# Performance work log

Measured on AMD Instinct MI355X. Metric: run time of the kernel, lower is better.

## Reference

```python
import jax, jax.numpy as jnp
import numpy as np

B, N, G = 4, 2000, 20            # images, proposals/img, gt boxes/img
C, P = 256, 7                    # ROIAlign output channels / pooled size
NUM_LABELS = 80
THR = 0.5                        # cfg.roi_threshold
NUM_SAMPLE = 512                 # cfg.roi_num_sample
POS_RATIO = 0.25                 # cfg.roi_positive_ratio
BETA = 1.0                       # cfg.smooth_l1_beta
IMG = 800.0


def _make_boxes(key, shape):
    k1, k2, k3, k4 = jax.random.split(key, 4)
    cx = jax.random.uniform(k1, shape) * IMG
    cy = jax.random.uniform(k2, shape) * IMG
    w = jax.random.uniform(k3, shape) * 192.0 + 8.0
    h = jax.random.uniform(k4, shape) * 192.0 + 8.0
    return jnp.stack([cx - w / 2, cy - h / 2, cx + w / 2, cy + h / 2], -1)


def setup_inputs() -> dict:
    key = jax.random.key(0)
    ks = jax.random.split(key, 8)
    feat_dim = C * P * P  # 12544
    return {
        "align_features": jax.random.normal(ks[0], (B * N, C, P, P), jnp.float32),
        "proposals": _make_boxes(ks[1], (B, N)),
        "gt_boxes": _make_boxes(ks[2], (B, G)),
        "gt_labels": jax.random.randint(ks[3], (B, G), 1, NUM_LABELS + 1),
        "W1": jax.random.normal(ks[4], (feat_dim, 1024), jnp.float32) * 0.01,
        "b1": jnp.zeros((1024,), jnp.float32),
        "W2": jax.random.normal(ks[5], (1024, 1024), jnp.float32) * 0.02,
        "b2": jnp.zeros((1024,), jnp.float32),
        "Wc": jax.random.normal(ks[6], (1024, NUM_LABELS + 1), jnp.float32) * 0.02,
        "bc": jnp.zeros((NUM_LABELS + 1,), jnp.float32),
        "Wb": jax.random.normal(ks[7], (1024, 4), jnp.float32) * 0.02,
        "bb": jnp.zeros((4,), jnp.float32),
    }


def _iou_matrix(p, g):
    # p: [B,N,4], g: [B,G,4] xyxy -> [B,N,G]
    x1 = jnp.maximum(p[:, :, None, 0], g[:, None, :, 0])
    y1 = jnp.maximum(p[:, :, None, 1], g[:, None, :, 1])
    x2 = jnp.minimum(p[:, :, None, 2], g[:, None, :, 2])
    y2 = jnp.minimum(p[:, :, None, 3], g[:, None, :, 3])
    inter = jnp.clip(x2 - x1, 0.0) * jnp.clip(y2 - y1, 0.0)
    ap = (p[..., 2] - p[..., 0]) * (p[..., 3] - p[..., 1])
    ag = (g[..., 2] - g[..., 0]) * (g[..., 3] - g[..., 1])
    return inter / (ap[:, :, None] + ag[:, None, :] - inter)


def _pos_to_delta(gt, p, posm):
    # Box.pos_to_delta; gt boxes are zeros for non-positives, so sanitize with posm
    pw = p[..., 2] - p[..., 0]
    ph = p[..., 3] - p[..., 1]
    pcx = p[..., 0] + 0.5 * pw
    pcy = p[..., 1] + 0.5 * ph
    gw = jnp.where(posm, gt[..., 2] - gt[..., 0], pw)
    gh = jnp.where(posm, gt[..., 3] - gt[..., 1], ph)
    gcx = jnp.where(posm, 0.5 * (gt[..., 0] + gt[..., 2]), pcx)
    gcy = jnp.where(posm, 0.5 * (gt[..., 1] + gt[..., 3]), pcy)
    dx = (gcx - pcx) / pw
    dy = (gcy - pcy) / ph
    dw = jnp.log(gw / pw)
    dh = jnp.log(gh / ph)
    return jnp.stack([dx, dy, dw, dh], -1)


def _forward(align_features, proposals, gt_boxes, gt_labels,
             W1, b1, W2, b2, Wc, bc, Wb, bb):
    # ---- labeling_proposals: IoU matrix + threshold assignment ----
    iou = _iou_matrix(proposals, gt_boxes)                 # [B,N,G]
    max_iou = iou.max(-1)
    match = iou.argmax(-1)                                 # [B,N]
    matched_lab = jnp.take_along_axis(gt_labels, match, 1)
    matched_box = jnp.take_along_axis(gt_boxes, match[..., None], 1)
    fg = max_iou > THR
    label = jnp.where(fg, matched_lab, 0)                  # [B,N]
    match_gt = jnp.where(fg[..., None], matched_box, 0.0)  # [B,N,4]

    # ---- sampling_proposals (deterministic first-k in place of randperm) ----
    num_pos = int(NUM_SAMPLE * POS_RATIO)
    num_neg = NUM_SAMPLE - num_pos
    pos = label >= 1
    neg = label == 0
    keep_p = pos & (jnp.cumsum(pos.astype(jnp.int32), 1) <= num_pos)
    keep_n = neg & (jnp.cumsum(neg.astype(jnp.int32), 1) <= num_neg)
    samp = jnp.where(keep_p, label, jnp.where(keep_n, 0, -1))  # [B,N]

    # ---- predict_scores_deltas: dense FC head ----
    x = align_features.reshape(B * N, -1)                  # [BN, 12544]
    h = jax.nn.relu(x @ W1 + b1)
    h = jax.nn.relu(h @ W2 + b2)
    probs = jax.nn.softmax(h @ Wc + bc, -1).reshape(B, N, -1)
    deltas = (h @ Wb + bb).reshape(B, N, 4)

    # ---- loss: NOTE original applies F.cross_entropy to already-softmaxed
    # scores (double softmax); replicated faithfully here. ----
    logp = jax.nn.log_softmax(probs, -1)
    tgt = jnp.clip(samp, 0)
    nll = -jnp.take_along_axis(logp, tgt[..., None], -1)[..., 0]
    valid = (samp >= 0).astype(probs.dtype)
    cls_loss = jnp.sum(nll * valid) / (B * NUM_SAMPLE)

    posm = samp > 0
    gt_d = _pos_to_delta(match_gt, proposals, posm)
    d = deltas - gt_d
    ad = jnp.abs(d)
    sl1 = jnp.where(ad < BETA, 0.5 * d * d / BETA, ad - 0.5 * BETA)
    loc_loss = jnp.sum(sl1 * posm[..., None].astype(sl1.dtype)) / (B * NUM_SAMPLE)
    return jnp.stack([cls_loss, loc_loss])


def reference(align_features, proposals, gt_boxes, gt_labels,
              W1, b1, W2, b2, Wc, bc, Wb, bb):
    return _forward(align_features, proposals, gt_boxes, gt_labels,
                    W1, b1, W2, b2, Wc, bc, Wb, bb)
```

## Files before the change

### kernel.cpp

```cpp
#include <hip/hip_runtime.h>
#include <hip/hip_bf16.h>
#include <stdint.h>

#define B_IMG 4
#define N_PROP 2000
#define G_GT 20
#define NPROP_TOT 8000
#define FEAT 12544
#define H_DIM 1024
#define NCLS 81
#define NCB 85
#define NCB_PAD 128
#define THR_IOU 0.5f
#define NUM_POS 128
#define NUM_NEG 384
#define M_SAMP 2048
#define SPLITK 4

typedef short bf16x8 __attribute__((ext_vector_type(8)));
typedef float f32x4 __attribute__((ext_vector_type(4)));

#define GLOBAL_AS __attribute__((address_space(1)))
#define LDS_AS __attribute__((address_space(3)))

__device__ __forceinline__ unsigned short f2bf(float f) {
    unsigned u = __float_as_uint(f);
    unsigned r = 0x7FFFu + ((u >> 16) & 1u);
    return (unsigned short)((u + r) >> 16);
}

__device__ __forceinline__ void async_lds16(void* lds, const void* g) {
    __builtin_amdgcn_global_load_lds((const GLOBAL_AS unsigned int*)g,
                                     (LDS_AS unsigned int*)lds, 16, 0, 0);
}

__global__ void k_sample(const float* __restrict__ prop, const float* __restrict__ gt,
                         const int* __restrict__ gtl,
                         int* __restrict__ sval, int* __restrict__ gidx,
                         float* __restrict__ gtdc, float* __restrict__ out2) {
    if (threadIdx.x == 0) { out2[0] = 0.f; out2[1] = 0.f; }
    int w = threadIdx.x >> 6;
    int lane = threadIdx.x & 63;
    for (int i = lane; i < 512; i += 64) { sval[w*512 + i] = -1; gidx[w*512 + i] = 0; }
    int run_p = 0, run_n = 0, run_s = 0;
    unsigned long long below = (1ull << lane) - 1ull;
    const float* gb_img = gt + (long)w * G_GT * 4;
    for (int c = 0; c < (N_PROP + 63) / 64; ++c) {
        int n = c * 64 + lane;
        int p = w * N_PROP + n;
        bool valid = n < N_PROP;
        int lab = 0, bi = 0;
        float px1=0, py1=0, px2=0, py2=0;
        if (valid) {
            const float* pr = prop + (long)p * 4;
            px1 = pr[0]; py1 = pr[1]; px2 = pr[2]; py2 = pr[3];
            float ap = (px2 - px1) * (py2 - py1);
            float best = -1.f;
            for (int g = 0; g < G_GT; ++g) {
                float gx1 = gb_img[g*4+0], gy1 = gb_img[g*4+1];
                float gx2 = gb_img[g*4+2], gy2 = gb_img[g*4+3];
                float iw = fmaxf(fminf(px2, gx2) - fmaxf(px1, gx1), 0.f);
                float ih = fmaxf(fminf(py2, gy2) - fmaxf(py1, gy1), 0.f);
                float inter = iw * ih;
                float ag = (gx2 - gx1) * (gy2 - gy1);
                float iou = inter / (ap + ag - inter);
                if (iou > best) { best = iou; bi = g; }
            }
            bool fg = best > THR_IOU;
            lab = fg ? gtl[w * G_GT + bi] : 0;
        }
        bool pos = valid && (lab >= 1);
        bool neg = valid && (lab == 0);
        unsigned long long mp = __ballot(pos);
        unsigned long long mn = __ballot(neg);
        int rp = run_p + __popcll(mp & below) + 1;
        int rn = run_n + __popcll(mn & below) + 1;
        int s = -1;
        if (pos && rp <= NUM_POS) s = lab;
        else if (neg && rn <= NUM_NEG) s = 0;
        run_p += __popcll(mp);
        run_n += __popcll(mn);
        bool sampled = s >= 0;
        unsigned long long ms = __ballot(sampled);
        int slot = w * 512 + run_s + __popcll(ms & below);
        run_s += __popcll(ms);
        if (sampled) {
            sval[slot] = s;
            gidx[slot] = p;
            if (s > 0) {
                const float* gb = gb_img + (long)bi * 4;
                float pw = px2 - px1, ph = py2 - py1;
                float pcx = px1 + 0.5f * pw, pcy = py1 + 0.5f * ph;
                float gw = gb[2] - gb[0], gh = gb[3] - gb[1];
                float gcx = 0.5f * (gb[0] + gb[2]), gcy = 0.5f * (gb[1] + gb[3]);
                gtdc[slot*4+0] = (gcx - pcx) / pw;
                gtdc[slot*4+1] = (gcy - pcy) / ph;
                gtdc[slot*4+2] = logf(gw / pw);
                gtdc[slot*4+3] = logf(gh / ph);
            }
        }
    }
}

__global__ void k_gather(const float* __restrict__ x, const int* __restrict__ gidx,
                         unsigned short* __restrict__ xg) {
    int row = blockIdx.x;
    const float* src = x + (long)gidx[row] * FEAT;
    unsigned short* dst = xg + (long)row * FEAT;
    for (int i = threadIdx.x * 4; i < FEAT; i += 1024) {
        float4 v = *(const float4*)(src + i);
        ushort4 o;
        o.x = f2bf(v.x); o.y = f2bf(v.y); o.z = f2bf(v.z); o.w = f2bf(v.w);
        *(ushort4*)(dst + i) = o;
    }
}

__global__ void k_transpose(const float* __restrict__ src, unsigned short* __restrict__ dst,
                            int K, int N) {
    __shared__ float tile[32][33];
    int k0 = blockIdx.x * 32;
    int n0 = blockIdx.y * 32;
    int tx = threadIdx.x & 31;
    int ty = threadIdx.x >> 5;
    for (int r = 0; r < 4; ++r)
        tile[ty + r * 8][tx] = src[(long)(k0 + ty + r * 8) * N + (n0 + tx)];
    __syncthreads();
    for (int r = 0; r < 4; ++r)
        dst[(long)(n0 + ty + r * 8) * K + (k0 + tx)] = f2bf(tile[tx][ty + r * 8]);
}

__global__ void k_build_wcb(const float* __restrict__ Wc, const float* __restrict__ bc,
                            const float* __restrict__ Wb, const float* __restrict__ bb,
                            unsigned short* __restrict__ WT, float* __restrict__ bias) {
    int idx = blockIdx.x * blockDim.x + threadIdx.x;
    if (idx >= NCB_PAD * H_DIM) return;
    int n = idx / H_DIM;
    int k = idx - n * H_DIM;
    float v = 0.f;
    if (n < NCLS) v = Wc[k * NCLS + n];
    else if (n < NCB) v = Wb[k * 4 + (n - NCLS)];
    WT[n * H_DIM + k] = f2bf(v);
    if (idx < NCB_PAD) {
        float bv = 0.f;
        if (idx < NCLS) bv = bc[idx];
        else if (idx < NCB) bv = bb[idx - NCLS];
        bias[idx] = bv;
    }
}

template<int TM, int OUT_MODE>
__global__ __launch_bounds__(256, 2)
void k_gemm(const unsigned short* __restrict__ A, const unsigned short* __restrict__ BT,
            const float* __restrict__ bias, void* __restrict__ Out,
            int M, int N, int K, int n_tiles_m, int n_tiles_n, int k_len) {
    __shared__ unsigned short As[TM * 32];
    __shared__ unsigned short Bs[128 * 32];
    const int t = threadIdx.x;
    int bid = blockIdx.x;
    const int tile_n = bid % n_tiles_n; bid /= n_tiles_n;
    const int tile_m = bid % n_tiles_m;
    const int ks = bid / n_tiles_m;
    const int m0 = tile_m * TM, n0 = tile_n * 128;
    const int w = t >> 6, lane = t & 63;
    const int wr = w >> 1, wc = w & 1;
    const int lm = lane & 15, quad = lane >> 4;
    const int rowt = t >> 2, seg = t & 3;
    const long kbase = (long)ks * k_len;

    const unsigned short* B_0 = BT + (long)(n0 + rowt) * K + kbase + seg * 8;
    const unsigned short* B_1 = BT + (long)(n0 + rowt + 64) * K + kbase + seg * 8;
    unsigned short* lB0 = &Bs[t * 8];
    unsigned short* lB1 = &Bs[(t + 256) * 8];

    const unsigned short* A_0 = nullptr;
    const unsigned short* A_1 = nullptr;
    unsigned short* lA0 = &As[t * 8];
    unsigned short* lA1 = nullptr;
    if constexpr (TM == 128) {
        A_0 = A + (long)(m0 + rowt) * K + kbase + seg * 8;
        A_1 = A + (long)(m0 + rowt + 64) * K + kbase + seg * 8;
        lA1 = &As[(t + 256) * 8];
    } else if constexpr (TM == 64) {
        A_0 = A + (long)(m0 + rowt) * K + kbase + seg * 8;
    } else {
        if (t < 128) A_0 = A + (long)(m0 + rowt) * K + kbase + seg * 8;
    }

    constexpr int MI = TM / 32;
    f32x4 acc[MI][4];
    for (int i = 0; i < MI; ++i)
        for (int j = 0; j < 4; ++j)
            for (int r = 0; r < 4; ++r) acc[i][j][r] = 0.f;

    const int KT = k_len >> 5;
    for (int kt = 0; kt < KT; ++kt) {
        async_lds16(lB0, B_0);
        async_lds16(lB1, B_1);
        B_0 += 32; B_1 += 32;
        if constexpr (TM == 128) {
            async_lds16(lA0, A_0); A_0 += 32;
            async_lds16(lA1, A_1); A_1 += 32;
        } else if constexpr (TM == 64) {
            async_lds16(lA0, A_0); A_0 += 32;
        } else {
            if (t < 128) { async_lds16(lA0, A_0); A_0 += 32; }
        }
        __syncthreads();
        bf16x8 af[MI], bfr[4];
        for (int i = 0; i < MI; ++i)
            af[i] = *(const bf16x8*)&As[(wr * (TM / 2) + i * 16 + lm) * 32 + quad * 8];
        for (int j = 0; j < 4; ++j)
            bfr[j] = *(const bf16x8*)&Bs[(wc * 64 + j * 16 + lm) * 32 + quad * 8];
        for (int i = 0; i < MI; ++i)
            for (int j = 0; j < 4; ++j)
                acc[i][j] = __builtin_amdgcn_mfma_f32_16x16x32_bf16(af[i], bfr[j], acc[i][j], 0, 0, 0);
        __syncthreads();
    }

    for (int i = 0; i < MI; ++i) {
        const int mbase = m0 + wr * (TM / 2) + i * 16 + quad * 4;
        for (int j = 0; j < 4; ++j) {
            const int n = n0 + wc * 64 + j * 16 + lm;
            float bv = 0.f;
            if constexpr (OUT_MODE != 0) bv = bias[n];
            for (int r = 0; r < 4; ++r) {
                const int m = mbase + r;
                float v = acc[i][j][r] + bv;
                if constexpr (OUT_MODE == 0) {
                    ((float*)Out)[((long)ks * M + m) * N + n] = v;
                } else if constexpr (OUT_MODE == 1) {
                    v = fmaxf(v, 0.f);
                    ((unsigned short*)Out)[(long)m * N + n] = f2bf(v);
                } else {
                    ((float*)Out)[(long)m * N + n] = v;
                }
            }
        }
    }
}

__global__ void k_reduce(const float* __restrict__ part, const float* __restrict__ b1,
                         unsigned short* __restrict__ h1) {
    const long MN = (long)M_SAMP * H_DIM;
    long i = ((long)blockIdx.x * 256 + threadIdx.x) * 4;
    float4 a = *(const float4*)(part + i);
    float4 b = *(const float4*)(part + MN + i);
    float4 c = *(const float4*)(part + 2 * MN + i);
    float4 d = *(const float4*)(part + 3 * MN + i);
    int col = (int)(i & (H_DIM - 1));
    float4 bv = *(const float4*)(b1 + col);
    ushort4 o;
    o.x = f2bf(fmaxf(a.x + b.x + c.x + d.x + bv.x, 0.f));
    o.y = f2bf(fmaxf(a.y + b.y + c.y + d.y + bv.y, 0.f));
    o.z = f2bf(fmaxf(a.z + b.z + c.z + d.z + bv.z, 0.f));
    o.w = f2bf(fmaxf(a.w + b.w + c.w + d.w + bv.w, 0.f));
    *(ushort4*)(h1 + i) = o;
}

__global__ void k_loss(const float* __restrict__ scores, const int* __restrict__ sval,
                       const float* __restrict__ gtdc, float* __restrict__ out2) {
    int i = blockIdx.x * blockDim.x + threadIdx.x;
    float cls = 0.f, loc = 0.f;
    int s = sval[i];
    if (s >= 0) {
        const float* sc = scores + (long)i * NCB_PAD;
        float mx = sc[0];
        for (int j = 1; j < NCLS; ++j) mx = fmaxf(mx, sc[j]);
        float sum = 0.f;
        for (int j = 0; j < NCLS; ++j) sum += __expf(sc[j] - mx);
        float inv = 1.f / sum;
        float m2 = -1e30f;
        for (int j = 0; j < NCLS; ++j)
            m2 = fmaxf(m2, __expf(sc[j] - mx) * inv);
        float s2 = 0.f, ptgt = 0.f;
        for (int j = 0; j < NCLS; ++j) {
            float pj = __expf(sc[j] - mx) * inv;
            s2 += __expf(pj - m2);
            if (j == s) ptgt = pj;
        }
        cls = m2 + __logf(s2) - ptgt;
        if (s > 0) {
            for (int j = 0; j < 4; ++j) {
                float d = sc[NCLS + j] - gtdc[i * 4 + j];
                float ad = fabsf(d);
                loc += (ad < 1.0f) ? 0.5f * d * d : ad - 0.5f;
            }
        }
    }
    for (int off = 32; off > 0; off >>= 1) {
        cls += __shfl_down(cls, off);
        loc += __shfl_down(loc, off);
    }
    __shared__ float scl[4], slo[4];
    int wv = threadIdx.x >> 6, lane = threadIdx.x & 63;
    if (lane == 0) { scl[wv] = cls; slo[wv] = loc; }
    __syncthreads();
    if (threadIdx.x == 0) {
        float c = scl[0] + scl[1] + scl[2] + scl[3];
        float l = slo[0] + slo[1] + slo[2] + slo[3];
        atomicAdd(&out2[0], c * (1.f / 2048.f));
        atomicAdd(&out2[1], l * (1.f / 2048.f));
    }
}

extern "C" void kernel_launch(void* const* d_in, const int* in_sizes, int n_in,
                              void* d_out, int out_size, void* d_ws, size_t ws_size,
                              hipStream_t stream) {
    const float* x    = (const float*)d_in[0];
    const float* prop = (const float*)d_in[1];
    const float* gt   = (const float*)d_in[2];
    const int*   gtl  = (const int*)d_in[3];
    const float* W1   = (const float*)d_in[4];
    const float* b1   = (const float*)d_in[5];
    const float* W2   = (const float*)d_in[6];
    const float* b2   = (const float*)d_in[7];
    const float* Wc   = (const float*)d_in[8];
    const float* bc   = (const float*)d_in[9];
    const float* Wb   = (const float*)d_in[10];
    const float* bb   = (const float*)d_in[11];
    float* out2 = (float*)d_out;
    (void)in_sizes; (void)n_in; (void)out_size; (void)ws_size;

    char* ws = (char*)d_ws;
    size_t off = 0;
    auto alloc = [&](size_t bytes) -> void* {
        void* p = ws + off;
        off += (bytes + 255) & ~(size_t)255;
        return p;
    };
    unsigned short* w1t    = (unsigned short*)alloc((size_t)H_DIM * FEAT * 2);
    unsigned short* w2t    = (unsigned short*)alloc((size_t)H_DIM * H_DIM * 2);
    unsigned short* wcbt   = (unsigned short*)alloc((size_t)NCB_PAD * H_DIM * 2);
    float*          biascb = (float*)alloc(NCB_PAD * 4);
    unsigned short* xg     = (unsigned short*)alloc((size_t)M_SAMP * FEAT * 2);
    float*          part   = (float*)alloc((size_t)SPLITK * M_SAMP * H_DIM * 4);
    unsigned short* h1     = (unsigned short*)alloc((size_t)M_SAMP * H_DIM * 2);
    unsigned short* h2     = (unsigned short*)alloc((size_t)M_SAMP * H_DIM * 2);
    float*          scores = (float*)alloc((size_t)M_SAMP * NCB_PAD * 4);
    int*            sval   = (int*)alloc(M_SAMP * 4);
    int*            gidx   = (int*)alloc(M_SAMP * 4);
    float*          gtdc   = (float*)alloc(M_SAMP * 16);

    k_sample<<<1, 256, 0, stream>>>(prop, gt, gtl, sval, gidx, gtdc, out2);
    k_transpose<<<dim3(FEAT / 32, H_DIM / 32), 256, 0, stream>>>(W1, w1t, FEAT, H_DIM);
    k_transpose<<<dim3(H_DIM / 32, H_DIM / 32), 256, 0, stream>>>(W2, w2t, H_DIM, H_DIM);
    k_build_wcb<<<(NCB_PAD * H_DIM + 255) / 256, 256, 0, stream>>>(Wc, bc, Wb, bb, wcbt, biascb);
    k_gather<<<M_SAMP, 256, 0, stream>>>(x, gidx, xg);

    k_gemm<128, 0><<<(M_SAMP / 128) * (H_DIM / 128) * SPLITK, 256, 0, stream>>>(
        xg, w1t, nullptr, part, M_SAMP, H_DIM, FEAT,
        M_SAMP / 128, H_DIM / 128, FEAT / SPLITK);
    k_reduce<<<(M_SAMP * H_DIM) / 1024, 256, 0, stream>>>(part, b1, h1);
    k_gemm<32, 1><<<(M_SAMP / 32) * (H_DIM / 128), 256, 0, stream>>>(
        h1, w2t, b2, h2, M_SAMP, H_DIM, H_DIM,
        M_SAMP / 32, H_DIM / 128, H_DIM);
    k_gemm<32, 2><<<(M_SAMP / 32) * 1, 256, 0, stream>>>(
        h2, wcbt, biascb, scores, M_SAMP, NCB_PAD, H_DIM,
        M_SAMP / 32, 1, H_DIM);
    k_loss<<<M_SAMP / 256, 256, 0, stream>>>(scores, sval, gtdc, out2);
}
```

Before: 762.2 us.

## Retune GEMM split-K and occupancy, reorder LDS staging layout, widen gather

Doubles split-K for the first FC GEMM and generalises the reduce kernel to loop over the partials. Raises launch bounds to four blocks per SM. Changes the global-to-LDS staging mapping so each wave's fragment is stored contiguously and can be read by lane index, aiming to cut LDS bank conflicts. Widens the gather loop to eight elements per thread. The higher split-K doubles partial-sum traffic, and the tighter launch bounds may force register spills.

```diff
diff --git a/kernel.cpp b/kernel.cpp
--- a/kernel.cpp
+++ b/kernel.cpp
@@ -15,7 +15,7 @@
 #define NUM_POS 128
 #define NUM_NEG 384
 #define M_SAMP 2048
-#define SPLITK 4
+#define SPLITK 8
 
 typedef short bf16x8 __attribute__((ext_vector_type(8)));
 typedef float f32x4 __attribute__((ext_vector_type(4)));
@@ -107,11 +107,14 @@
     int row = blockIdx.x;
     const float* src = x + (long)gidx[row] * FEAT;
     unsigned short* dst = xg + (long)row * FEAT;
-    for (int i = threadIdx.x * 4; i < FEAT; i += 1024) {
-        float4 v = *(const float4*)(src + i);
-        ushort4 o;
-        o.x = f2bf(v.x); o.y = f2bf(v.y); o.z = f2bf(v.z); o.w = f2bf(v.w);
-        *(ushort4*)(dst + i) = o;
+    for (int i = threadIdx.x * 8; i < FEAT; i += 2048) {
+        float4 v0 = *(const float4*)(src + i);
+        float4 v1 = *(const float4*)(src + i + 4);
+        ushort4 o0, o1;
+        o0.x = f2bf(v0.x); o0.y = f2bf(v0.y); o0.z = f2bf(v0.z); o0.w = f2bf(v0.w);
+        o1.x = f2bf(v1.x); o1.y = f2bf(v1.y); o1.z = f2bf(v1.z); o1.w = f2bf(v1.w);
+        *(ushort4*)(dst + i) = o0;
+        *(ushort4*)(dst + i + 4) = o1;
     }
 }
 
@@ -149,7 +152,7 @@
 }
 
 template<int TM, int OUT_MODE>
-__global__ __launch_bounds__(256, 2)
+__global__ __launch_bounds__(256, 4)
 void k_gemm(const unsigned short* __restrict__ A, const unsigned short* __restrict__ BT,
             const float* __restrict__ bias, void* __restrict__ Out,
             int M, int N, int K, int n_tiles_m, int n_tiles_n, int k_len) {
@@ -164,11 +167,13 @@
     const int w = t >> 6, lane = t & 63;
     const int wr = w >> 1, wc = w & 1;
     const int lm = lane & 15, quad = lane >> 4;
-    const int rowt = t >> 2, seg = t & 3;
     const long kbase = (long)ks * k_len;
 
-    const unsigned short* B_0 = BT + (long)(n0 + rowt) * K + kbase + seg * 8;
-    const unsigned short* B_1 = BT + (long)(n0 + rowt + 64) * K + kbase + seg * 8;
+    const int srow = ((t >> 6) << 4) | (t & 15);
+    const int sseg = (t >> 4) & 3;
+
+    const unsigned short* B_0 = BT + (long)(n0 + srow) * K + kbase + sseg * 8;
+    const unsigned short* B_1 = BT + (long)(n0 + srow + 64) * K + kbase + sseg * 8;
     unsigned short* lB0 = &Bs[t * 8];
     unsigned short* lB1 = &Bs[(t + 256) * 8];
 
@@ -177,13 +182,13 @@
     unsigned short* lA0 = &As[t * 8];
     unsigned short* lA1 = nullptr;
     if constexpr (TM == 128) {
-        A_0 = A + (long)(m0 + rowt) * K + kbase + seg * 8;
-        A_1 = A + (long)(m0 + rowt + 64) * K + kbase + seg * 8;
+        A_0 = A + (long)(m0 + srow) * K + kbase + sseg * 8;
+        A_1 = A + (long)(m0 + srow + 64) * K + kbase + sseg * 8;
         lA1 = &As[(t + 256) * 8];
     } else if constexpr (TM == 64) {
-        A_0 = A + (long)(m0 + rowt) * K + kbase + seg * 8;
+        A_0 = A + (long)(m0 + srow) * K + kbase + sseg * 8;
     } else {
-        if (t < 128) A_0 = A + (long)(m0 + rowt) * K + kbase + seg * 8;
+        if (t < 128) A_0 = A + (long)(m0 + srow) * K + kbase + sseg * 8;
     }
 
     constexpr int MI = TM / 32;
@@ -208,9 +213,9 @@
         __syncthreads();
         bf16x8 af[MI], bfr[4];
         for (int i = 0; i < MI; ++i)
-            af[i] = *(const bf16x8*)&As[(wr * (TM / 2) + i * 16 + lm) * 32 + quad * 8];
+            af[i] = *(const bf16x8*)&As[((wr * MI + i) * 64 + lane) * 8];
         for (int j = 0; j < 4; ++j)
-            bfr[j] = *(const bf16x8*)&Bs[(wc * 64 + j * 16 + lm) * 32 + quad * 8];
+            bfr[j] = *(const bf16x8*)&Bs[((wc * 4 + j) * 64 + lane) * 8];
         for (int i = 0; i < MI; ++i)
             for (int j = 0; j < 4; ++j)
                 acc[i][j] = __builtin_amdgcn_mfma_f32_16x16x32_bf16(af[i], bfr[j], acc[i][j], 0, 0, 0);
@@ -243,17 +248,18 @@
                          unsigned short* __restrict__ h1) {
     const long MN = (long)M_SAMP * H_DIM;
     long i = ((long)blockIdx.x * 256 + threadIdx.x) * 4;
-    float4 a = *(const float4*)(part + i);
-    float4 b = *(const float4*)(part + MN + i);
-    float4 c = *(const float4*)(part + 2 * MN + i);
-    float4 d = *(const float4*)(part + 3 * MN + i);
+    float4 s = *(const float4*)(part + i);
+    for (int k = 1; k < SPLITK; ++k) {
+        float4 v = *(const float4*)(part + (long)k * MN + i);
+        s.x += v.x; s.y += v.y; s.z += v.z; s.w += v.w;
+    }
     int col = (int)(i & (H_DIM - 1));
     float4 bv = *(const float4*)(b1 + col);
     ushort4 o;
-    o.x = f2bf(fmaxf(a.x + b.x + c.x + d.x + bv.x, 0.f));
-    o.y = f2bf(fmaxf(a.y + b.y + c.y + d.y + bv.y, 0.f));
-    o.z = f2bf(fmaxf(a.z + b.z + c.z + d.z + bv.z, 0.f));
-    o.w = f2bf(fmaxf(a.w + b.w + c.w + d.w + bv.w, 0.f));
+    o.x = f2bf(fmaxf(s.x + bv.x, 0.f));
+    o.y = f2bf(fmaxf(s.y + bv.y, 0.f));
+    o.z = f2bf(fmaxf(s.z + bv.z, 0.f));
+    o.w = f2bf(fmaxf(s.w + bv.w, 0.f));
     *(ushort4*)(h1 + i) = o;
 }
 
```

New measurement: 804.7 us. 5.6% more time.
